# Optimization experiments

Hardware: AMD Instinct MI355X
Metric: run time of the kernel (lower is better)

Reference implementation:

```python
import jax, jax.numpy as jnp
import numpy as np

TEMPLATE_SZ = 7
MAX_SR = 3


def setup_inputs() -> dict:
    key = jax.random.key(0)
    # image-like values in [0, 255) since the module ends with a uint8 cast
    x = jax.random.uniform(key, (2, 1, 192, 192), dtype=jnp.float32) * 255.0
    return {"inputs": x, "search_range": 3}


def reference(inputs, search_range):
    # Equivalent math to: pad(max_sr) -> unfold(k, pad=k//2) -> unfold(s) ->
    # permute -> slice sub-window -> reshape -> uint8.
    # Both zero-pads commute, so fold them into one pad and gather directly,
    # avoiding the huge duplicated double-im2col intermediate.
    k = TEMPLATE_SZ
    max_sr = MAX_SR
    cv = 2 * search_range + 1          # cost_volume_sz
    offset = max_sr - search_range
    B, C, H, W = inputs.shape          # C == 1 (implied by the torch view)
    pad = max_sr + k // 2              # combined zero padding
    Q = jnp.pad(inputs[:, 0].astype(jnp.float32), ((0, 0), (pad, pad), (pad, pad)))
    r = offset + jnp.arange(cv)        # search offsets within max window
    t = jnp.arange(k)                  # template offsets
    # windows[b,i,j,dy,dx,ty,tx] = Q[b, i + r[dy] + ty, j + r[dx] + tx]
    iy = jnp.arange(H)[:, None, None] + r[None, :, None] + t[None, None, :]  # [H, cv, k]
    jx = jnp.arange(W)[:, None, None] + r[None, :, None] + t[None, None, :]  # [W, cv, k]
    win = Q[:, iy[:, None, :, None, :, None], jx[None, :, None, :, None, :]]  # [B,H,W,cv,cv,k,k]
    return win.reshape(B, H, W, cv * cv, k * k).astype(jnp.uint8)
```

## Files before the change

kernel.cpp:

```cpp
#include <hip/hip_runtime.h>


#define KT 7
#define K2 49
#define MAX_SR 3
#define B_ 2
#define H_ 192
#define W_ 192
#define PAD 6
#define PX 48
#define PCOLS (PX + 2*PAD)
#define PSTRIDE 61
#define PROWS 13
#define NTHREADS 256
#define RMAX 10
#define NG (PX / 4)

typedef int vint4 __attribute__((ext_vector_type(4)));

__global__ __launch_bounds__(NTHREADS) void esw_kernel(
    const float* __restrict__ in, int* __restrict__ out,
    int cv, int offset, int d , int cvmagic )
{
    __shared__ int sw[1024];

    const int tid = threadIdx.x;
    const int w0 = blockIdx.x * PX;
    const int h  = blockIdx.y;
    const int b  = blockIdx.z;

    const float* inb = in + b * (H_ * W_);
    for (int i = tid; i < PROWS * PCOLS; i += NTHREADS) {
        int dy = i / PCOLS;
        int dx = i - dy * PCOLS;
        int y = h + dy - PAD;
        int x = w0 + dx - PAD;
        int v = 0;
        if ((unsigned)y < (unsigned)H_ && (unsigned)x < (unsigned)W_)
            v = (int)inb[y * W_ + x];
        int c = dy * PSTRIDE + dx;
        sw[c + (c >> 2)] = v;
    }

    int fe[RMAX][4];
    #pragma unroll
    for (int r = 0; r < RMAX; ++r) {
        int j4 = 4 * (tid + NTHREADS * r);
        #pragma unroll
        for (int u = 0; u < 4; ++u) {
            int jj = j4 + u;
            if (jj >= 4 * d) jj = 4 * d - 1;
            int p_in = (jj >= d) + (jj >= 2 * d) + (jj >= 3 * d);
            int j  = jj - p_in * d;
            int rr = j / K2;
            int tt = j - rr * K2;
            int ry = (rr * cvmagic) >> 16;
            int rx = rr - ry * cv;
            int ty = tt / KT;
            int tx = tt - ty * KT;
            int e = (offset + ry + ty) * PSTRIDE + (offset + rx + tx) + p_in;
            fe[r][u] = e + (e >> 2);
        }
    }
    __syncthreads();

    long long p0 = (long long)(b * H_ + h) * W_ + w0;
    int* op = out + p0 * (long long)d;

    #pragma unroll
    for (int r = 0; r < RMAX; ++r) {
        int q = tid + NTHREADS * r;
        if (q < d) {
            int* oq = op + 4 * q;
            #pragma unroll
            for (int g = 0; g < NG; g += 2) {
                vint4 a, c2;
                a.x  = sw[fe[r][0] + 5 * g];
                c2.x = sw[fe[r][0] + 5 * g + 5];
                a.y  = sw[fe[r][1] + 5 * g];
                c2.y = sw[fe[r][1] + 5 * g + 5];
                a.z  = sw[fe[r][2] + 5 * g];
                c2.z = sw[fe[r][2] + 5 * g + 5];
                a.w  = sw[fe[r][3] + 5 * g];
                c2.w = sw[fe[r][3] + 5 * g + 5];
                *(vint4*)(oq + (long long)g * 4 * d)       = a;
                *(vint4*)(oq + (long long)(g + 1) * 4 * d) = c2;
            }
        }
    }
}

extern "C" void kernel_launch(void* const* d_in, const int* in_sizes, int n_in,
                              void* d_out, int out_size, void* d_ws, size_t ws_size,
                              hipStream_t stream) {
    const float* in = (const float*)d_in[0];
    int* out = (int*)d_out;

    int cv2 = out_size / (B_ * H_ * W_ * K2);
    int cv = 1;
    while (cv * cv < cv2) ++cv;
    int offset = MAX_SR - (cv - 1) / 2;
    int d = cv2 * K2;
    int cvmagic = 65536 / cv + 1;

    dim3 grid(W_ / PX, H_, B_);
    esw_kernel<<<grid, NTHREADS, 0, stream>>>(in, out, cv, offset, d, cvmagic);
}
```

Before: 724.8 us.

## Use persistent blocks writing contiguous 4-pixel output groups from small patch

Replaces the per-row 48-pixel tile grid with a fixed grid of 768 persistent blocks, each looping over groups of 4 consecutive pixels. Each block loads a 13x16 patch into shared memory per group and writes one fully contiguous output chunk, instead of strided stores spread across 48 pixels. This aims for better write coalescing and fewer blocks. In exchange it adds a barrier-synchronised small patch reload per iteration and reuses each loaded patch much less.

```diff
diff --git a/kernel.cpp b/kernel.cpp
--- a/kernel.cpp
+++ b/kernel.cpp
@@ -7,14 +7,13 @@
 #define B_ 2
 #define H_ 192
 #define W_ 192
+#define HW (H_ * W_)
 #define PAD 6
-#define PX 48
-#define PCOLS (PX + 2*PAD)
-#define PSTRIDE 61
-#define PROWS 13
 #define NTHREADS 256
 #define RMAX 10
-#define NG (PX / 4)
+#define PS 17
+#define NBLOCKS 768
+#define NGROUPS (B_ * H_ * W_ / 4)
 
 typedef int vint4 __attribute__((ext_vector_type(4)));
 
@@ -22,25 +21,10 @@
     const float* __restrict__ in, int* __restrict__ out,
     int cv, int offset, int d , int cvmagic )
 {
-    __shared__ int sw[1024];
+    __shared__ int patch[13 * PS + 4];
 
     const int tid = threadIdx.x;
-    const int w0 = blockIdx.x * PX;
-    const int h  = blockIdx.y;
-    const int b  = blockIdx.z;
-
-    const float* inb = in + b * (H_ * W_);
-    for (int i = tid; i < PROWS * PCOLS; i += NTHREADS) {
-        int dy = i / PCOLS;
-        int dx = i - dy * PCOLS;
-        int y = h + dy - PAD;
-        int x = w0 + dx - PAD;
-        int v = 0;
-        if ((unsigned)y < (unsigned)H_ && (unsigned)x < (unsigned)W_)
-            v = (int)inb[y * W_ + x];
-        int c = dy * PSTRIDE + dx;
-        sw[c + (c >> 2)] = v;
-    }
+    const int bid = blockIdx.x;
 
     int fe[RMAX][4];
     #pragma unroll
@@ -58,33 +42,42 @@
             int rx = rr - ry * cv;
             int ty = tt / KT;
             int tx = tt - ty * KT;
-            int e = (offset + ry + ty) * PSTRIDE + (offset + rx + tx) + p_in;
-            fe[r][u] = e + (e >> 2);
+            fe[r][u] = (offset + ry + ty) * PS + (offset + rx + tx) + p_in;
         }
     }
-    __syncthreads();
 
-    long long p0 = (long long)(b * H_ + h) * W_ + w0;
-    int* op = out + p0 * (long long)d;
+    for (int it = 0; it < NGROUPS / NBLOCKS; ++it) {
+        const int g = it * NBLOCKS + bid;
+        const int pix0 = 4 * g;
+        const int b   = pix0 / HW;
+        const int rem = pix0 - b * HW;
+        const int h   = rem / W_;
+        const int w   = rem - h * W_;
 
-    #pragma unroll
-    for (int r = 0; r < RMAX; ++r) {
-        int q = tid + NTHREADS * r;
-        if (q < d) {
-            int* oq = op + 4 * q;
-            #pragma unroll
-            for (int g = 0; g < NG; g += 2) {
-                vint4 a, c2;
-                a.x  = sw[fe[r][0] + 5 * g];
-                c2.x = sw[fe[r][0] + 5 * g + 5];
-                a.y  = sw[fe[r][1] + 5 * g];
-                c2.y = sw[fe[r][1] + 5 * g + 5];
-                a.z  = sw[fe[r][2] + 5 * g];
-                c2.z = sw[fe[r][2] + 5 * g + 5];
-                a.w  = sw[fe[r][3] + 5 * g];
-                c2.w = sw[fe[r][3] + 5 * g + 5];
-                *(vint4*)(oq + (long long)g * 4 * d)       = a;
-                *(vint4*)(oq + (long long)(g + 1) * 4 * d) = c2;
+        __syncthreads();
+        if (tid < 13 * 16) {
+            int dy = tid >> 4;
+            int dx = tid & 15;
+            int y = h + dy - PAD;
+            int x = w + dx - PAD;
+            int v = 0;
+            if ((unsigned)y < (unsigned)H_ && (unsigned)x < (unsigned)W_)
+                v = (int)in[b * HW + y * W_ + x];
+            patch[dy * PS + dx] = v;
+        }
+        __syncthreads();
+
+        int* op = out + (long long)g * (long long)(4 * d);
+        #pragma unroll
+        for (int r = 0; r < RMAX; ++r) {
+            int q = tid + NTHREADS * r;
+            if (q < d) {
+                vint4 v;
+                v.x = patch[fe[r][0]];
+                v.y = patch[fe[r][1]];
+                v.z = patch[fe[r][2]];
+                v.w = patch[fe[r][3]];
+                *(vint4*)(op + 4 * q) = v;
             }
         }
     }
@@ -103,6 +96,5 @@
     int d = cv2 * K2;
     int cvmagic = 65536 / cv + 1;
 
-    dim3 grid(W_ / PX, H_, B_);
-    esw_kernel<<<grid, NTHREADS, 0, stream>>>(in, out, cv, offset, d, cvmagic);
+    esw_kernel<<<NBLOCKS, NTHREADS, 0, stream>>>(in, out, cv, offset, d, cvmagic);
 }
```

Result: faster. 705.0 us (-2.7%).
